# Optimization experiments

Measured on AMD Instinct MI355X. Metric: run time of the kernel, lower is better.

The kernel has to match this reference:

```python
import jax, jax.numpy as jnp
import numpy as np

HID = 2048      # hidden_size
NH = 32         # num_heads
G = 8           # num_kv_groups
R = NH // G     # repeat factor (heads per kv group)
HD = HID // NH  # head_dim = 64
SCALE = HD ** 0.5


def setup_inputs() -> dict:
    key = jax.random.key(0)
    ks = jax.random.split(key, 10)
    B, S = 2, 1024
    x = jax.random.normal(ks[0], (B, S, HID), dtype=jnp.float32)
    attention_mask = jnp.ones((B, S, S), dtype=jnp.float32)
    # Linear params stored as [in, out] (y = x @ W + b), same math as torch Linear.
    Wq = jax.random.normal(ks[1], (HID, HID), dtype=jnp.float32) * 0.02
    bq = jnp.zeros((HID,), dtype=jnp.float32)
    Wk = jax.random.normal(ks[2], (HID, G * HD), dtype=jnp.float32) * 0.02
    bk = jnp.zeros((G * HD,), dtype=jnp.float32)
    Wv = jax.random.normal(ks[3], (HID, G * HD), dtype=jnp.float32) * 0.02
    bv = jnp.zeros((G * HD,), dtype=jnp.float32)
    Wo = jax.random.normal(ks[4], (HID, HID), dtype=jnp.float32) * 0.02
    bo = jnp.zeros((HID,), dtype=jnp.float32)
    return {"x": x, "attention_mask": attention_mask,
            "Wq": Wq, "bq": bq, "Wk": Wk, "bk": bk,
            "Wv": Wv, "bv": bv, "Wo": Wo, "bo": bo}


def reference(x, attention_mask, Wq, bq, Wk, bk, Wv, bv, Wo, bo):
    B, S, _ = x.shape
    # Projections. Group heads as (G, R) instead of repeat_interleave:
    # repeat_interleave(key, R, dim=2) duplicates each kv group R times, which is
    # exactly sharing key[:, :, g] across the R heads of group g.
    q = (x @ Wq + bq).reshape(B, S, G, R, HD)   # [B,S,G,R,HD] (heads = G*R in order)
    k = (x @ Wk + bk).reshape(B, S, G, HD)      # [B,S,G,HD]
    v = (x @ Wv + bv).reshape(B, S, G, HD)
    # scores [B,G,R,Sq,Sk] == torch's [B, NH, Sq, Sk] with NH = G*R
    scores = jnp.einsum('bqgrd,bkgd->bgrqk', q, k) / SCALE
    scores = scores * attention_mask[:, None, None]  # multiplicative mask per head
    w = jax.nn.softmax(scores, axis=-1)
    out = jnp.einsum('bgrqk,bkgd->bqgrd', w, v).reshape(B, S, HID)
    return out @ Wo + bo + x
```

## Files before the change

### kernel.cpp

```cpp
#include <hip/hip_runtime.h>

typedef unsigned short u16;
typedef unsigned int u32;
typedef __attribute__((ext_vector_type(8))) short bf16x8;
typedef __attribute__((ext_vector_type(4))) float f32x4;

#define HID 2048
#define S_LEN 1024
#define BATCH 2
#define G_KV 8
#define R_REP 4
#define HD 64
#define NQKV 3072

__device__ __forceinline__ u16 f2bf(float f) {
    union { u32 u; float ff; } x; x.ff = f;
    u32 u = x.u;
    u += 0x7FFFu + ((u >> 16) & 1u);
    return (u16)(u >> 16);
}

__device__ __forceinline__ void gload_lds16(const void* g, void* l) {
    __builtin_amdgcn_global_load_lds((const __attribute__((address_space(1))) void*)g,
                                     (__attribute__((address_space(3))) void*)l,
                                     16, 0, 0);
}

__global__ __launch_bounds__(256) void cvt_x(const float* __restrict__ in,
                                             u16* __restrict__ out) {
    int i = (blockIdx.x * 256 + threadIdx.x) * 8;
    float4 a = *(const float4*)(in + i);
    float4 b = *(const float4*)(in + i + 4);
    u16 t[8] = {f2bf(a.x), f2bf(a.y), f2bf(a.z), f2bf(a.w),
                f2bf(b.x), f2bf(b.y), f2bf(b.z), f2bf(b.w)};
    *(uint4*)(out + i) = *(const uint4*)t;
}

__global__ __launch_bounds__(256) void transpose_cvt(const float* __restrict__ in,
                                                     u16* __restrict__ out,
                                                     int K, int N) {
    __shared__ float tile[32][33];
    int n0 = blockIdx.x * 32, k0 = blockIdx.y * 32;
    int tx = threadIdx.x, ty = threadIdx.y;
#pragma unroll
    for (int j = 0; j < 4; ++j)
        tile[ty + j * 8][tx] = in[(size_t)(k0 + ty + j * 8) * N + n0 + tx];
    __syncthreads();
#pragma unroll
    for (int j = 0; j < 4; ++j)
        out[(size_t)(n0 + ty + j * 8) * K + k0 + tx] = f2bf(tile[tx][ty + j * 8]);
}

__global__ __launch_bounds__(256) void gemm_qkv(const u16* __restrict__ Xb,
                                                const u16* __restrict__ WT,
                                                const float* __restrict__ bq,
                                                const float* __restrict__ bk,
                                                const float* __restrict__ bv,
                                                u16* __restrict__ qb,
                                                u16* __restrict__ kb,
                                                u16* __restrict__ vb) {
    __shared__ __align__(16) u16 As[128 * 32];
    __shared__ __align__(16) u16 Bs[128 * 32];
    int tid = threadIdx.x;
    int w = tid >> 6, lane = tid & 63, quad = lane >> 4, l16 = lane & 15;
    int m0 = blockIdx.y * 128, n0 = blockIdx.x * 128;
    int wr = (w >> 1) * 64, wc = (w & 1) * 64;
    int srow = lane >> 2, scol = (lane & 3) * 8;

    f32x4 acc[4][4];
#pragma unroll
    for (int i = 0; i < 4; ++i)
#pragma unroll
        for (int j = 0; j < 4; ++j) acc[i][j] = (f32x4){0.f, 0.f, 0.f, 0.f};

    for (int k0 = 0; k0 < 2048; k0 += 32) {
#pragma unroll
        for (int c = 0; c < 2; ++c) {
            int row = c * 64 + w * 16 + srow;
            gload_lds16(&Xb[(size_t)(m0 + row) * 2048 + k0 + scol], &As[(c * 64 + w * 16) * 32]);
            gload_lds16(&WT[(size_t)(n0 + row) * 2048 + k0 + scol], &Bs[(c * 64 + w * 16) * 32]);
        }
        __syncthreads();
        bf16x8 af[4], bfr[4];
#pragma unroll
        for (int mt = 0; mt < 4; ++mt)
            af[mt] = *(const bf16x8*)&As[(wr + mt * 16 + l16) * 32 + quad * 8];
#pragma unroll
        for (int nt = 0; nt < 4; ++nt)
            bfr[nt] = *(const bf16x8*)&Bs[(wc + nt * 16 + l16) * 32 + quad * 8];
#pragma unroll
        for (int mt = 0; mt < 4; ++mt)
#pragma unroll
            for (int nt = 0; nt < 4; ++nt)
                acc[mt][nt] = __builtin_amdgcn_mfma_f32_16x16x32_bf16(af[mt], bfr[nt], acc[mt][nt], 0, 0, 0);
        __syncthreads();
    }

#pragma unroll
    for (int nt = 0; nt < 4; ++nt) {
        int n = n0 + wc + nt * 16 + l16;
        float bias;
        if (n < 2048) bias = bq[n];
        else if (n < 2560) bias = bk[n - 2048];
        else bias = bv[n - 2560];
#pragma unroll
        for (int mt = 0; mt < 4; ++mt) {
#pragma unroll
            for (int reg = 0; reg < 4; ++reg) {
                int m = m0 + wr + mt * 16 + quad * 4 + reg;
                float val = acc[mt][nt][reg] + bias;
                int b = m >> 10, s = m & 1023;
                u16 bfv = f2bf(val);
                if (n < 2048) {
                    int g = n >> 8, r = (n >> 6) & 3, d = n & 63;
                    qb[((((size_t)(b * G_KV + g) * R_REP + r) * S_LEN) + s) * HD + d] = bfv;
                } else if (n < 2560) {
                    int n2 = n - 2048, g = n2 >> 6, d = n2 & 63;
                    kb[(((size_t)(b * G_KV + g) * S_LEN) + s) * HD + d] = bfv;
                } else {
                    int n2 = n - 2560, g = n2 >> 6, d = n2 & 63;
                    vb[(((size_t)(b * G_KV + g) * HD + d) * S_LEN) + s] = bfv;
                }
            }
        }
    }
}

__global__ __launch_bounds__(256) void attn_mfma(const u16* __restrict__ qbuf,
                                                 const u16* __restrict__ kbuf,
                                                 const u16* __restrict__ vtbuf,
                                                 const float* __restrict__ mask,
                                                 u16* __restrict__ aout) {
    __shared__ __align__(16) u16 Ks[64 * 72];
    __shared__ __align__(16) u16 Vs[64 * 72];
    __shared__ __align__(16) float Ms[64 * 68];
    __shared__ __align__(16) u16 Ps[64 * 72];

    int bid = blockIdx.x;
    int qblk = bid & 15, r = (bid >> 4) & 3, g = (bid >> 6) & 7, b = bid >> 9;
    int tid = threadIdx.x;
    int w = tid >> 6, lane = tid & 63, quad = lane >> 4, l16 = lane & 15;
    int s0 = qblk * 64;

    const u16* qrow = qbuf +
        ((((size_t)(b * G_KV + g) * R_REP + r) * S_LEN) + s0 + w * 16 + l16) * HD;
    bf16x8 qf0 = *(const bf16x8*)(qrow + quad * 8);
    bf16x8 qf1 = *(const bf16x8*)(qrow + 32 + quad * 8);

    f32x4 o_acc[4];
#pragma unroll
    for (int i = 0; i < 4; ++i) o_acc[i] = (f32x4){0.f, 0.f, 0.f, 0.f};
    float l_tot[4] = {0.f, 0.f, 0.f, 0.f};

    const u16* kbase  = kbuf  + (size_t)(b * G_KV + g) * S_LEN * HD;
    const u16* vtbase = vtbuf + (size_t)(b * G_KV + g) * HD * S_LEN;
    const float* mbase = mask + ((size_t)b * S_LEN + s0) * S_LEN;

    int srow = tid >> 2, sc = (tid & 3) * 16;
    int prow = w * 16 + quad * 4;

    for (int kt = 0; kt < 16; ++kt) {
        __syncthreads();
        {
            const u16* kr = kbase + (size_t)(kt * 64 + srow) * HD + sc;
            *(uint4*)&Ks[srow * 72 + sc]     = *(const uint4*)kr;
            *(uint4*)&Ks[srow * 72 + sc + 8] = *(const uint4*)(kr + 8);
            const u16* vr = vtbase + (size_t)srow * S_LEN + kt * 64 + sc;
            *(uint4*)&Vs[srow * 72 + sc]     = *(const uint4*)vr;
            *(uint4*)&Vs[srow * 72 + sc + 8] = *(const uint4*)(vr + 8);
            const float* mr = mbase + (size_t)srow * S_LEN + kt * 64 + sc;
#pragma unroll
            for (int i = 0; i < 4; ++i) {
                float4 m4 = *(const float4*)(mr + i * 4);
                Ms[srow * 68 + sc + i * 4 + 0] = m4.x * 0.125f;
                Ms[srow * 68 + sc + i * 4 + 1] = m4.y * 0.125f;
                Ms[srow * 68 + sc + i * 4 + 2] = m4.z * 0.125f;
                Ms[srow * 68 + sc + i * 4 + 3] = m4.w * 0.125f;
            }
        }
        __syncthreads();

        f32x4 p[4];
#pragma unroll
        for (int nt = 0; nt < 4; ++nt) {
            bf16x8 kf0 = *(const bf16x8*)&Ks[(nt * 16 + l16) * 72 + quad * 8];
            bf16x8 kf1 = *(const bf16x8*)&Ks[(nt * 16 + l16) * 72 + 32 + quad * 8];
            f32x4 z = (f32x4){0.f, 0.f, 0.f, 0.f};
            z = __builtin_amdgcn_mfma_f32_16x16x32_bf16(qf0, kf0, z, 0, 0, 0);
            p[nt] = __builtin_amdgcn_mfma_f32_16x16x32_bf16(qf1, kf1, z, 0, 0, 0);
        }

        float part[4] = {0.f, 0.f, 0.f, 0.f};
#pragma unroll
        for (int nt = 0; nt < 4; ++nt) {
#pragma unroll
            for (int reg = 0; reg < 4; ++reg) {
                int qr = prow + reg;
                float e = __expf(p[nt][reg] * Ms[qr * 68 + nt * 16 + l16]);
                part[reg] += e;
                Ps[qr * 72 + nt * 16 + l16] = f2bf(e);
            }
        }
        __syncthreads();

#pragma unroll
        for (int reg = 0; reg < 4; ++reg) {
            float v = part[reg];
            v += __shfl_xor(v, 1);
            v += __shfl_xor(v, 2);
            v += __shfl_xor(v, 4);
            v += __shfl_xor(v, 8);
            l_tot[reg] += v;
        }

        bf16x8 pf0 = *(const bf16x8*)&Ps[(w * 16 + l16) * 72 + quad * 8];
        bf16x8 pf1 = *(const bf16x8*)&Ps[(w * 16 + l16) * 72 + 32 + quad * 8];
#pragma unroll
        for (int nt = 0; nt < 4; ++nt) {
            bf16x8 vf0 = *(const bf16x8*)&Vs[(nt * 16 + l16) * 72 + quad * 8];
            bf16x8 vf1 = *(const bf16x8*)&Vs[(nt * 16 + l16) * 72 + 32 + quad * 8];
            o_acc[nt] = __builtin_amdgcn_mfma_f32_16x16x32_bf16(pf0, vf0, o_acc[nt], 0, 0, 0);
            o_acc[nt] = __builtin_amdgcn_mfma_f32_16x16x32_bf16(pf1, vf1, o_acc[nt], 0, 0, 0);
        }
    }

#pragma unroll
    for (int reg = 0; reg < 4; ++reg) {
        int row = prow + reg;
        float inv = 1.0f / l_tot[reg];
        int sidx = s0 + row;
        u16* dst = aout + ((size_t)(b * S_LEN + sidx)) * HID + (g * R_REP + r) * HD;
#pragma unroll
        for (int nt = 0; nt < 4; ++nt)
            dst[nt * 16 + l16] = f2bf(o_acc[nt][reg] * inv);
    }
}

__global__ __launch_bounds__(256) void gemm_o(const u16* __restrict__ A,
                                              const u16* __restrict__ WT,
                                              const float* __restrict__ bo,
                                              const float* __restrict__ Xres,
                                              float* __restrict__ out) {
    __shared__ __align__(16) u16 As[128 * 32];
    __shared__ __align__(16) u16 Bs[128 * 32];
    int tid = threadIdx.x;
    int w = tid >> 6, lane = tid & 63, quad = lane >> 4, l16 = lane & 15;
    int m0 = blockIdx.y * 128, n0 = blockIdx.x * 128;
    int wr = (w >> 1) * 64, wc = (w & 1) * 64;
    int srow = lane >> 2, scol = (lane & 3) * 8;

    f32x4 acc[4][4];
#pragma unroll
    for (int i = 0; i < 4; ++i)
#pragma unroll
        for (int j = 0; j < 4; ++j) acc[i][j] = (f32x4){0.f, 0.f, 0.f, 0.f};

    for (int k0 = 0; k0 < 2048; k0 += 32) {
#pragma unroll
        for (int c = 0; c < 2; ++c) {
            int row = c * 64 + w * 16 + srow;
            gload_lds16(&A[(size_t)(m0 + row) * 2048 + k0 + scol],  &As[(c * 64 + w * 16) * 32]);
            gload_lds16(&WT[(size_t)(n0 + row) * 2048 + k0 + scol], &Bs[(c * 64 + w * 16) * 32]);
        }
        __syncthreads();
        bf16x8 af[4], bfr[4];
#pragma unroll
        for (int mt = 0; mt < 4; ++mt)
            af[mt] = *(const bf16x8*)&As[(wr + mt * 16 + l16) * 32 + quad * 8];
#pragma unroll
        for (int nt = 0; nt < 4; ++nt)
            bfr[nt] = *(const bf16x8*)&Bs[(wc + nt * 16 + l16) * 32 + quad * 8];
#pragma unroll
        for (int mt = 0; mt < 4; ++mt)
#pragma unroll
            for (int nt = 0; nt < 4; ++nt)
                acc[mt][nt] = __builtin_amdgcn_mfma_f32_16x16x32_bf16(af[mt], bfr[nt], acc[mt][nt], 0, 0, 0);
        __syncthreads();
    }

#pragma unroll
    for (int nt = 0; nt < 4; ++nt) {
        int n = n0 + wc + nt * 16 + l16;
        float bias = bo[n];
#pragma unroll
        for (int mt = 0; mt < 4; ++mt) {
#pragma unroll
            for (int reg = 0; reg < 4; ++reg) {
                int m = m0 + wr + mt * 16 + quad * 4 + reg;
                out[(size_t)m * 2048 + n] = acc[mt][nt][reg] + bias + Xres[(size_t)m * 2048 + n];
            }
        }
    }
}

extern "C" void kernel_launch(void* const* d_in, const int* in_sizes, int n_in,
                              void* d_out, int out_size, void* d_ws, size_t ws_size,
                              hipStream_t stream) {
    const float* x    = (const float*)d_in[0];
    const float* mask = (const float*)d_in[1];
    const float* Wq   = (const float*)d_in[2];
    const float* bq   = (const float*)d_in[3];
    const float* Wk   = (const float*)d_in[4];
    const float* bk   = (const float*)d_in[5];
    const float* Wv   = (const float*)d_in[6];
    const float* bv   = (const float*)d_in[7];
    const float* Wo   = (const float*)d_in[8];
    const float* bo   = (const float*)d_in[9];
    float* out = (float*)d_out;

    u16* ws = (u16*)d_ws;
    size_t off = 0;
    u16* WqkvT = ws + off; off += (size_t)NQKV * 2048;
    u16* WoT   = ws + off; off += (size_t)2048 * 2048;
    u16* q_buf = ws + off; off += (size_t)BATCH * G_KV * R_REP * S_LEN * HD;
    u16* k_buf = ws + off; off += (size_t)BATCH * G_KV * S_LEN * HD;
    u16* v_buf = ws + off; off += (size_t)BATCH * G_KV * S_LEN * HD;
    u16* a_out = ws + off; off += (size_t)2048 * 2048;
    u16* Xb    = a_out;

    cvt_x<<<dim3(2048 * 2048 / (256 * 8)), 256, 0, stream>>>(x, Xb);

    dim3 tb(32, 8);
    transpose_cvt<<<dim3(64, 64), tb, 0, stream>>>(Wq, WqkvT, 2048, 2048);
    transpose_cvt<<<dim3(16, 64), tb, 0, stream>>>(Wk, WqkvT + (size_t)2048 * 2048, 2048, 512);
    transpose_cvt<<<dim3(16, 64), tb, 0, stream>>>(Wv, WqkvT + (size_t)2560 * 2048, 2048, 512);
    transpose_cvt<<<dim3(64, 64), tb, 0, stream>>>(Wo, WoT, 2048, 2048);

    gemm_qkv<<<dim3(NQKV / 128, 2048 / 128), 256, 0, stream>>>(Xb, WqkvT, bq, bk, bv,
                                                               q_buf, k_buf, v_buf);

    attn_mfma<<<dim3(BATCH * G_KV * R_REP * (S_LEN / 64)), 256, 0, stream>>>(
        q_buf, k_buf, v_buf, mask, a_out);

    gemm_o<<<dim3(2048 / 128, 2048 / 128), 256, 0, stream>>>(a_out, WoT, bo, x, out);
}
```

Measured before the change: 284.7 us.

## Prefetch attention tiles into registers, bf16 mask, fold scale into Q, XCD-aware block mapping

The attention kernel now loads the next K/V/mask tile into registers while computing the current one, which overlaps global loads with MFMA and softmax work. The fp32 mask is converted once to bf16 in a separate pass that reuses the WqkvT workspace, halving mask traffic and LDS footprint inside attention. The 1/sqrt(d) scale moves into the Q projection epilogue, and the block index is remapped so that blocks sharing a (batch, group) land on the same XCD for L2 reuse. The extra conversion pass adds a full read and write of the mask, and rounding the mask to bf16 loses precision for arbitrary mask values.

```diff
diff --git a/kernel.cpp b/kernel.cpp
--- a/kernel.cpp
+++ b/kernel.cpp
@@ -18,6 +18,9 @@
     u32 u = x.u;
     u += 0x7FFFu + ((u >> 16) & 1u);
     return (u16)(u >> 16);
+}
+__device__ __forceinline__ float bf2f(u16 v) {
+    union { u32 u; float f; } x; x.u = ((u32)v) << 16; return x.f;
 }
 
 __device__ __forceinline__ void gload_lds16(const void* g, void* l) {
@@ -110,16 +113,15 @@
                 int m = m0 + wr + mt * 16 + quad * 4 + reg;
                 float val = acc[mt][nt][reg] + bias;
                 int b = m >> 10, s = m & 1023;
-                u16 bfv = f2bf(val);
                 if (n < 2048) {
                     int g = n >> 8, r = (n >> 6) & 3, d = n & 63;
-                    qb[((((size_t)(b * G_KV + g) * R_REP + r) * S_LEN) + s) * HD + d] = bfv;
+                    qb[((((size_t)(b * G_KV + g) * R_REP + r) * S_LEN) + s) * HD + d] = f2bf(val * 0.125f);
                 } else if (n < 2560) {
                     int n2 = n - 2048, g = n2 >> 6, d = n2 & 63;
-                    kb[(((size_t)(b * G_KV + g) * S_LEN) + s) * HD + d] = bfv;
+                    kb[(((size_t)(b * G_KV + g) * S_LEN) + s) * HD + d] = f2bf(val);
                 } else {
                     int n2 = n - 2560, g = n2 >> 6, d = n2 & 63;
-                    vb[(((size_t)(b * G_KV + g) * HD + d) * S_LEN) + s] = bfv;
+                    vb[(((size_t)(b * G_KV + g) * HD + d) * S_LEN) + s] = f2bf(val);
                 }
             }
         }
@@ -129,15 +131,19 @@
 __global__ __launch_bounds__(256) void attn_mfma(const u16* __restrict__ qbuf,
                                                  const u16* __restrict__ kbuf,
                                                  const u16* __restrict__ vtbuf,
-                                                 const float* __restrict__ mask,
+                                                 const u16* __restrict__ mask_bf,
                                                  u16* __restrict__ aout) {
     __shared__ __align__(16) u16 Ks[64 * 72];
     __shared__ __align__(16) u16 Vs[64 * 72];
-    __shared__ __align__(16) float Ms[64 * 68];
+    __shared__ __align__(16) u16 Ms[64 * 72];
     __shared__ __align__(16) u16 Ps[64 * 72];
 
-    int bid = blockIdx.x;
-    int qblk = bid & 15, r = (bid >> 4) & 3, g = (bid >> 6) & 7, b = bid >> 9;
+    int d = blockIdx.x;
+    int xcd = d & 7, j = d >> 3;
+    int pr = xcd * 2 + (j >> 6);
+    int r = (j >> 4) & 3, qblk = j & 15;
+    int b = pr >> 3, g = pr & 7;
+
     int tid = threadIdx.x;
     int w = tid >> 6, lane = tid & 63, quad = lane >> 4, l16 = lane & 15;
     int s0 = qblk * 64;
@@ -154,31 +160,40 @@
 
     const u16* kbase  = kbuf  + (size_t)(b * G_KV + g) * S_LEN * HD;
     const u16* vtbase = vtbuf + (size_t)(b * G_KV + g) * HD * S_LEN;
-    const float* mbase = mask + ((size_t)b * S_LEN + s0) * S_LEN;
+    const u16* mbase  = mask_bf + ((size_t)b * S_LEN + s0) * S_LEN;
 
     int srow = tid >> 2, sc = (tid & 3) * 16;
     int prow = w * 16 + quad * 4;
 
+    uint4 kp0, kp1, vp0, vp1, mp0, mp1;
+    {
+        const u16* kr = kbase + (size_t)srow * HD + sc;
+        kp0 = *(const uint4*)kr; kp1 = *(const uint4*)(kr + 8);
+        const u16* vr = vtbase + (size_t)srow * S_LEN + sc;
+        vp0 = *(const uint4*)vr; vp1 = *(const uint4*)(vr + 8);
+        const u16* mr = mbase + (size_t)srow * S_LEN + sc;
+        mp0 = *(const uint4*)mr; mp1 = *(const uint4*)(mr + 8);
+    }
+
     for (int kt = 0; kt < 16; ++kt) {
         __syncthreads();
-        {
-            const u16* kr = kbase + (size_t)(kt * 64 + srow) * HD + sc;
-            *(uint4*)&Ks[srow * 72 + sc]     = *(const uint4*)kr;
-            *(uint4*)&Ks[srow * 72 + sc + 8] = *(const uint4*)(kr + 8);
-            const u16* vr = vtbase + (size_t)srow * S_LEN + kt * 64 + sc;
-            *(uint4*)&Vs[srow * 72 + sc]     = *(const uint4*)vr;
-            *(uint4*)&Vs[srow * 72 + sc + 8] = *(const uint4*)(vr + 8);
-            const float* mr = mbase + (size_t)srow * S_LEN + kt * 64 + sc;
-#pragma unroll
-            for (int i = 0; i < 4; ++i) {
-                float4 m4 = *(const float4*)(mr + i * 4);
-                Ms[srow * 68 + sc + i * 4 + 0] = m4.x * 0.125f;
-                Ms[srow * 68 + sc + i * 4 + 1] = m4.y * 0.125f;
-                Ms[srow * 68 + sc + i * 4 + 2] = m4.z * 0.125f;
-                Ms[srow * 68 + sc + i * 4 + 3] = m4.w * 0.125f;
-            }
-        }
-        __syncthreads();
+        *(uint4*)&Ks[srow * 72 + sc]     = kp0;
+        *(uint4*)&Ks[srow * 72 + sc + 8] = kp1;
+        *(uint4*)&Vs[srow * 72 + sc]     = vp0;
+        *(uint4*)&Vs[srow * 72 + sc + 8] = vp1;
+        *(uint4*)&Ms[srow * 72 + sc]     = mp0;
+        *(uint4*)&Ms[srow * 72 + sc + 8] = mp1;
+        __syncthreads();
+
+        if (kt < 15) {
+            int nk = (kt + 1) * 64;
+            const u16* kr = kbase + (size_t)(nk + srow) * HD + sc;
+            kp0 = *(const uint4*)kr; kp1 = *(const uint4*)(kr + 8);
+            const u16* vr = vtbase + (size_t)srow * S_LEN + nk + sc;
+            vp0 = *(const uint4*)vr; vp1 = *(const uint4*)(vr + 8);
+            const u16* mr = mbase + (size_t)srow * S_LEN + nk + sc;
+            mp0 = *(const uint4*)mr; mp1 = *(const uint4*)(mr + 8);
+        }
 
         f32x4 p[4];
 #pragma unroll
@@ -196,7 +211,8 @@
 #pragma unroll
             for (int reg = 0; reg < 4; ++reg) {
                 int qr = prow + reg;
-                float e = __expf(p[nt][reg] * Ms[qr * 68 + nt * 16 + l16]);
+                float m = bf2f(Ms[qr * 72 + nt * 16 + l16]);
+                float e = __expf(p[nt][reg] * m);
                 part[reg] += e;
                 Ps[qr * 72 + nt * 16 + l16] = f2bf(e);
             }
@@ -316,7 +332,8 @@
     u16* k_buf = ws + off; off += (size_t)BATCH * G_KV * S_LEN * HD;
     u16* v_buf = ws + off; off += (size_t)BATCH * G_KV * S_LEN * HD;
     u16* a_out = ws + off; off += (size_t)2048 * 2048;
-    u16* Xb    = a_out;
+    u16* Xb      = a_out;
+    u16* mask_bf = WqkvT;
 
     cvt_x<<<dim3(2048 * 2048 / (256 * 8)), 256, 0, stream>>>(x, Xb);
 
@@ -329,8 +346,10 @@
     gemm_qkv<<<dim3(NQKV / 128, 2048 / 128), 256, 0, stream>>>(Xb, WqkvT, bq, bk, bv,
                                                                q_buf, k_buf, v_buf);
 
+    cvt_x<<<dim3(BATCH * S_LEN * S_LEN / (256 * 8)), 256, 0, stream>>>(mask, mask_bf);
+
     attn_mfma<<<dim3(BATCH * G_KV * R_REP * (S_LEN / 64)), 256, 0, stream>>>(
-        q_buf, k_buf, v_buf, mask, a_out);
+        q_buf, k_buf, v_buf, mask_bf, a_out);
 
     gemm_o<<<dim3(2048 / 128, 2048 / 128), 256, 0, stream>>>(a_out, WoT, bo, x, out);
 }
```

Measured after the change: 273.0 us. 4.1% less time.
